# Kernel tuning notes

Measured on AMD Instinct MI355X. Metric: run time of the kernel, lower is better.

## Reference

```python
import jax, jax.numpy as jnp
import numpy as np

N_NODES = 100000
N_EDGES = 3200000
IN_FEATS = 16
OUT_FEATS = 2
K = 3


def setup_inputs() -> dict:
    key = jax.random.key(0)
    k1, k2, k3, k4 = jax.random.split(key, 4)
    in_feat = jax.random.normal(k1, (N_NODES, IN_FEATS), dtype=jnp.float32)
    # Linear(K*in_feats -> out_feats, bias=False) weight, torch layout (out, in)
    W = jax.random.normal(k2, (OUT_FEATS, K * IN_FEATS), dtype=jnp.float32) * (1.0 / np.sqrt(K * IN_FEATS))
    src = jax.random.randint(k3, (N_EDGES,), 0, N_NODES, dtype=jnp.int64)
    dst = jax.random.randint(k4, (N_EDGES,), 0, N_NODES, dtype=jnp.int64)
    # cached dgl.laplacian_lambda_max value; 2.0 is the normalized-Laplacian bound
    lambda_max = jnp.full((1,), 2.0, dtype=jnp.float32)
    return {"in_feat": in_feat, "W": W, "src": src, "dst": dst, "lambda_max": lambda_max}


def reference(in_feat, W, src, dst, lambda_max):
    N = in_feat.shape[0]
    # in-degree based symmetric normalization, clamp(min=1)
    deg = jax.ops.segment_sum(jnp.ones_like(dst, dtype=in_feat.dtype), dst, num_segments=N)
    norm = jnp.clip(deg, 1.0) ** -0.5  # (N,)
    norm = norm[:, None]
    re_norm = (2.0 / lambda_max)[None, :]  # (1,1), broadcasts over nodes

    def prop(x):
        # D^{-1/2} A D^{-1/2} x via gather from src, scatter-sum to dst
        m = (x * norm)[src]                                    # (E, d)
        return jax.ops.segment_sum(m, dst, num_segments=N) * norm

    X0 = in_feat
    X1 = -re_norm * prop(X0) + X0 * (re_norm - 1.0)
    X2 = -2.0 * re_norm * prop(X1) + X1 * (2.0 * (re_norm - 1.0)) - X0
    Xt = jnp.concatenate([X0, X1, X2], axis=1)                 # (N, K*d)
    h = Xt @ W.T                                               # (N, out)
    return jax.nn.relu(h)  # DGL ChebConv default activation
```

## Files before the change

kernel.cpp:

```cpp
#include <hip/hip_runtime.h>
#include <hip/hip_bf16.h>


#define NN   100000
#define NE   3200000
#define F    16
#define CB   128
#define NBUK 782
#define ECHK 8192
#define NBLK 391
#define LCAP 5120
#define HXW  1025

__device__ __forceinline__ float bflo(unsigned int u) {
    return __uint_as_float(u << 16);
}
__device__ __forceinline__ float bfhi(unsigned int u) {
    return __uint_as_float(u & 0xffff0000u);
}
__device__ __forceinline__ unsigned int f2bf(float f) {
    __hip_bfloat16 b = __float2bfloat16(f);
    return (unsigned int)*reinterpret_cast<unsigned short*>(&b);
}

__global__ __launch_bounds__(512) void k_lsort(const int* __restrict__ src,
        const int* __restrict__ dst, int* __restrict__ H, int* __restrict__ hxg,
        int* __restrict__ csort) {
    __shared__ int pk[ECHK];
    __shared__ int hx[HXW];
    __shared__ int cur[1024];
    __shared__ int csum[512];
    int t = threadIdx.x, blk = blockIdx.x;
    for (int j = t; j < 1024; j += 512) hx[j] = 0;
    __syncthreads();
    int s0 = blk * ECHK;
    int lim = min(s0 + ECHK, NE);
    for (int e = s0 + t; e < lim; e += 512)
        atomicAdd(&hx[dst[e] >> 7], 1);
    __syncthreads();
    int b0 = t * 2;
    int c0 = hx[b0], c1 = hx[b0 + 1];
    if (b0 < NBUK)     H[blk * NBUK + b0]     = c0;
    if (b0 + 1 < NBUK) H[blk * NBUK + b0 + 1] = c1;
    csum[t] = c0 + c1;
    __syncthreads();
    for (int o = 1; o < 512; o <<= 1) {
        int add = (t >= o) ? csum[t - o] : 0;
        __syncthreads();
        csum[t] += add;
        __syncthreads();
    }
    int ce = csum[t] - (c0 + c1);
    hx[b0] = ce;  hx[b0 + 1] = ce + c0;
    cur[b0] = ce; cur[b0 + 1] = ce + c0;
    if (t == 511) hx[1024] = csum[511];
    __syncthreads();
    for (int j = t; j < HXW; j += 512)
        hxg[blk * HXW + j] = hx[j];
    for (int e = s0 + t; e < lim; e += 512) {
        int d = dst[e];
        int pos = atomicAdd(&cur[d >> 7], 1);
        pk[pos] = (src[e] << 7) | (d & 127);
    }
    __syncthreads();
    int len = lim - s0;
    for (int i = t; i < len; i += 512)
        csort[s0 + i] = pk[i];
}

__global__ void k_colscan(int* __restrict__ H, int* __restrict__ T) {
    __shared__ int tmp[512];
    int b = blockIdx.x, t = threadIdx.x;
    int v = (t < NBLK) ? H[t * NBUK + b] : 0;
    tmp[t] = v;
    __syncthreads();
    for (int o = 1; o < 512; o <<= 1) {
        int add = (t >= o) ? tmp[t - o] : 0;
        __syncthreads();
        tmp[t] += add;
        __syncthreads();
    }
    if (t < NBLK) H[t * NBUK + b] = tmp[t] - v;
    if (t == 0) T[b] = tmp[511];
}

__global__ void k_basescan(const int* __restrict__ T, int* __restrict__ base) {
    __shared__ int tmp[1024];
    int t = threadIdx.x;
    int v = (t < NBUK) ? T[t] : 0;
    tmp[t] = v;
    __syncthreads();
    for (int o = 1; o < 1024; o <<= 1) {
        int add = (t >= o) ? tmp[t - o] : 0;
        __syncthreads();
        tmp[t] += add;
        __syncthreads();
    }
    if (t < NBUK) base[t] = tmp[t] - v;
    if (t == 0) base[NBUK] = tmp[1023];
}

__global__ __launch_bounds__(256) void k_sort(const int* __restrict__ csort,
        const int* __restrict__ H, const int* __restrict__ hxg,
        const int* __restrict__ base, const float* __restrict__ X0,
        int* __restrict__ es, int* __restrict__ node_off,
        float* __restrict__ norm, unsigned short* __restrict__ Y0) {
    __shared__ int pk[LCAP];
    __shared__ int cnt[CB], loc[CB], cur[CB];
    __shared__ float nvs[CB];
    int b = blockIdx.x, t = threadIdx.x;
    int beg = base[b], end = base[b + 1];
    int len = end - beg;
    if (len > LCAP) len = LCAP;
    if (t < CB) cnt[t] = 0;
    if (b == 0 && t < F) Y0[(size_t)NN * F + t] = 0;
    __syncthreads();
    for (int c = t; c < NBLK; c += 256) {
        int h0 = hxg[c * HXW + b];
        int h1 = hxg[c * HXW + b + 1];
        int dpos = H[c * NBUK + b];
        int rl = h1 - h0;
        if (dpos >= LCAP) continue;
        if (dpos + rl > LCAP) rl = LCAP - dpos;
        int sbase = c * ECHK + h0;
        for (int i = 0; i < rl; ++i)
            pk[dpos + i] = csort[sbase + i];
    }
    __syncthreads();
    for (int i = t; i < len; i += 256)
        atomicAdd(&cnt[pk[i] & 127], 1);
    __syncthreads();
    if (t < CB) loc[t] = cnt[t];
    __syncthreads();
    for (int o = 1; o < CB; o <<= 1) {
        int add = 0;
        if (t < CB && t >= o) add = loc[t - o];
        __syncthreads();
        if (t < CB) loc[t] += add;
        __syncthreads();
    }
    if (t < CB) {
        int excl = loc[t] - cnt[t];
        loc[t] = excl;
        cur[t] = 0;
        int n = b * CB + t;
        if (n <= NN) node_off[n] = beg + excl;
        if (n < NN) {
            int c = cnt[t];
            float nv = rsqrtf((float)(c < 1 ? 1 : c));
            norm[n] = nv;
            nvs[t] = nv;
        }
    }
    __syncthreads();
    for (int j = t; j < CB * F; j += 256) {
        int dl = j >> 4;
        int n = b * CB + dl;
        if (n < NN) {
            size_t gidx = (size_t)n * F + (j & 15);
            Y0[gidx] = (unsigned short)f2bf(X0[gidx] * nvs[dl]);
        }
    }
    for (int i = t; i < len; i += 256) {
        int p = pk[i];
        int dl = p & 127;
        int pos = beg + loc[dl] + atomicAdd(&cur[dl], 1);
        es[pos] = p >> 7;
    }
}

__global__ __launch_bounds__(256) void k_prop1(const int* __restrict__ off,
        const int* __restrict__ es, const unsigned short* __restrict__ Y0,
        const float* __restrict__ X0, const float* __restrict__ norm,
        const float* __restrict__ lm, unsigned short* __restrict__ Y1) {
    int tid = blockIdx.x * 256 + threadIdx.x;
    if (tid < 4) ((uint2*)Y1)[(size_t)NN * 4 + tid] = make_uint2(0u, 0u);
    int n = tid >> 2, h = tid & 3;
    if (n >= NN) return;
    int beg = off[n], end = off[n + 1];
    const uint2* Yv = (const uint2*)Y0;
    float a0 = 0.f, a1 = 0.f, a2 = 0.f, a3 = 0.f;
    int e0 = beg;
    int c = end - e0;
    int iA = (h < c)     ? es[e0 + h]     : NN;
    int iB = (4 + h < c) ? es[e0 + 4 + h] : NN;
    while (e0 < end) {
        int e1 = e0 + 8;
        int c1 = end - e1;
        int nA = (h < c1)     ? es[e1 + h]     : NN;
        int nB = (4 + h < c1) ? es[e1 + 4 + h] : NN;
#pragma unroll
        for (int j = 0; j < 4; ++j) {
            int s = __shfl(iA, j, 4);
            uint2 u = Yv[(size_t)s * 4 + h];
            a0 += bflo(u.x); a1 += bfhi(u.x);
            a2 += bflo(u.y); a3 += bfhi(u.y);
        }
#pragma unroll
        for (int j = 0; j < 4; ++j) {
            int s = __shfl(iB, j, 4);
            uint2 u = Yv[(size_t)s * 4 + h];
            a0 += bflo(u.x); a1 += bfhi(u.x);
            a2 += bflo(u.y); a3 += bfhi(u.y);
        }
        iA = nA; iB = nB; e0 = e1;
    }
    float r  = 2.0f / lm[0];
    float nv = norm[n];
    float k1 = -r * nv, k2 = r - 1.0f;
    float4 x0 = ((const float4*)X0)[tid];
    float x1a = k1 * a0 + k2 * x0.x;
    float x1b = k1 * a1 + k2 * x0.y;
    float x1c = k1 * a2 + k2 * x0.z;
    float x1d = k1 * a3 + k2 * x0.w;
    uint2 o;
    o.x = f2bf(nv * x1a) | (f2bf(nv * x1b) << 16);
    o.y = f2bf(nv * x1c) | (f2bf(nv * x1d) << 16);
    ((uint2*)Y1)[tid] = o;
}

__global__ __launch_bounds__(256) void k_prop2(const int* __restrict__ off,
        const int* __restrict__ es, const unsigned short* __restrict__ Y1,
        const float* __restrict__ X0, const float* __restrict__ norm,
        const float* __restrict__ lm, const float* __restrict__ W,
        float* __restrict__ out) {
    __shared__ float Ws[96];
    if (threadIdx.x < 96) Ws[threadIdx.x] = W[threadIdx.x];
    __syncthreads();
    int tid = blockIdx.x * 256 + threadIdx.x;
    int n = tid >> 2, h = tid & 3;
    if (n >= NN) return;
    int beg = off[n], end = off[n + 1];
    const uint2* Yv = (const uint2*)Y1;
    float a0 = 0.f, a1 = 0.f, a2 = 0.f, a3 = 0.f;
    int e0 = beg;
    int c = end - e0;
    int iA = (h < c)     ? es[e0 + h]     : NN;
    int iB = (4 + h < c) ? es[e0 + 4 + h] : NN;
    while (e0 < end) {
        int e1 = e0 + 8;
        int c1 = end - e1;
        int nA = (h < c1)     ? es[e1 + h]     : NN;
        int nB = (4 + h < c1) ? es[e1 + 4 + h] : NN;
#pragma unroll
        for (int j = 0; j < 4; ++j) {
            int s = __shfl(iA, j, 4);
            uint2 u = Yv[(size_t)s * 4 + h];
            a0 += bflo(u.x); a1 += bfhi(u.x);
            a2 += bflo(u.y); a3 += bfhi(u.y);
        }
#pragma unroll
        for (int j = 0; j < 4; ++j) {
            int s = __shfl(iB, j, 4);
            uint2 u = Yv[(size_t)s * 4 + h];
            a0 += bflo(u.x); a1 += bfhi(u.x);
            a2 += bflo(u.y); a3 += bfhi(u.y);
        }
        iA = nA; iB = nB; e0 = e1;
    }
    float r  = 2.0f / lm[0];
    float nv = norm[n];
    float rn = 1.0f / nv;
    float4 x0 = ((const float4*)X0)[tid];
    uint2 uy = ((const uint2*)Y1)[tid];
    float x1a = bflo(uy.x) * rn, x1b = bfhi(uy.x) * rn;
    float x1c = bflo(uy.y) * rn, x1d = bfhi(uy.y) * rn;
    float c1 = -2.0f * r * nv, c2 = 2.0f * (r - 1.0f);
    float x2a = c1 * a0 + c2 * x1a - x0.x;
    float x2b = c1 * a1 + c2 * x1b - x0.y;
    float x2c = c1 * a2 + c2 * x1c - x0.z;
    float x2d = c1 * a3 + c2 * x1d - x0.w;
    int f0 = 4 * h;
    float t0 = Ws[f0] * x0.x + Ws[f0 + 1] * x0.y + Ws[f0 + 2] * x0.z + Ws[f0 + 3] * x0.w
             + Ws[16 + f0] * x1a + Ws[17 + f0] * x1b + Ws[18 + f0] * x1c + Ws[19 + f0] * x1d
             + Ws[32 + f0] * x2a + Ws[33 + f0] * x2b + Ws[34 + f0] * x2c + Ws[35 + f0] * x2d;
    float t1 = Ws[48 + f0] * x0.x + Ws[49 + f0] * x0.y + Ws[50 + f0] * x0.z + Ws[51 + f0] * x0.w
             + Ws[64 + f0] * x1a + Ws[65 + f0] * x1b + Ws[66 + f0] * x1c + Ws[67 + f0] * x1d
             + Ws[80 + f0] * x2a + Ws[81 + f0] * x2b + Ws[82 + f0] * x2c + Ws[83 + f0] * x2d;
    t0 += __shfl_xor(t0, 2, 4); t0 += __shfl_xor(t0, 1, 4);
    t1 += __shfl_xor(t1, 2, 4); t1 += __shfl_xor(t1, 1, 4);
    if (h == 0) {
        out[(size_t)n * 2 + 0] = fmaxf(t0, 0.f);
        out[(size_t)n * 2 + 1] = fmaxf(t1, 0.f);
    }
}

extern "C" void kernel_launch(void* const* d_in, const int* in_sizes, int n_in,
                              void* d_out, int out_size, void* d_ws, size_t ws_size,
                              hipStream_t stream) {
    const float* X0  = (const float*)d_in[0];
    const float* W   = (const float*)d_in[1];
    const int*   src = (const int*)d_in[2];
    const int*   dst = (const int*)d_in[3];
    const float* lm  = (const float*)d_in[4];
    float* out = (float*)d_out;

    int*   H        = (int*)d_ws;
    int*   hxg      = H + (size_t)NBLK * NBUK;
    int*   T        = hxg + (size_t)NBLK * HXW;
    int*   base     = T + NBUK;
    int*   csort    = base + (NBUK + 1);
    int*   es       = csort + NE;
    int*   node_off = es + NE;
    float* norm     = (float*)(node_off + (NN + 1));
    unsigned short* Y0 = (unsigned short*)(norm + NN);
    unsigned short* Y1 = Y0 + (size_t)(NN + 1) * F;

    const int gridP = (NN * 4 + 255) / 256;

    k_lsort   <<<NBLK, 512, 0, stream>>>(src, dst, H, hxg, csort);
    k_colscan <<<NBUK, 512, 0, stream>>>(H, T);
    k_basescan<<<1, 1024, 0, stream>>>(T, base);
    k_sort    <<<NBUK, 256, 0, stream>>>(csort, H, hxg, base, X0, es, node_off, norm, Y0);
    k_prop1   <<<gridP, 256, 0, stream>>>(node_off, es, Y0, X0, norm, lm, Y1);
    k_prop2   <<<gridP, 256, 0, stream>>>(node_off, es, Y1, X0, norm, lm, W, out);
}
```

Measured before the change: 196.8 us.

## Fuse bucket sort with first propagation and drop global base scan

Removes the global base scan by giving each destination bucket a fixed LCAP-sized slot in the edge array, and packs each node's offset and degree into one word. Degrees are now counted with global atomics during the local sort, so a separate k_norm kernel can build Y0 before the sort. The first propagation is fused into the per-bucket sort kernel and reads sorted indices straight from shared memory. The second propagation stages each half-bucket's edge indices in shared memory. The trade-offs are 3.2M global atomics on deg, an extra memset and launch, a larger padded es array, and degree clamped to 1023 in the packed word.

Result: slower. 318.8 us (+62.0%).

```diff
diff --git a/kernel.cpp b/kernel.cpp
--- a/kernel.cpp
+++ b/kernel.cpp
@@ -11,6 +11,7 @@
 #define NBLK 391
 #define LCAP 5120
 #define HXW  1025
+#define PCAP 4608
 
 __device__ __forceinline__ float bflo(unsigned int u) {
     return __uint_as_float(u << 16);
@@ -25,7 +26,7 @@
 
 __global__ __launch_bounds__(512) void k_lsort(const int* __restrict__ src,
         const int* __restrict__ dst, int* __restrict__ H, int* __restrict__ hxg,
-        int* __restrict__ csort) {
+        int* __restrict__ csort, int* __restrict__ deg) {
     __shared__ int pk[ECHK];
     __shared__ int hx[HXW];
     __shared__ int cur[1024];
@@ -35,8 +36,11 @@
     __syncthreads();
     int s0 = blk * ECHK;
     int lim = min(s0 + ECHK, NE);
-    for (int e = s0 + t; e < lim; e += 512)
-        atomicAdd(&hx[dst[e] >> 7], 1);
+    for (int e = s0 + t; e < lim; e += 512) {
+        int d = dst[e];
+        atomicAdd(&hx[d >> 7], 1);
+        atomicAdd(&deg[d], 1);
+    }
     __syncthreads();
     int b0 = t * 2;
     int c0 = hx[b0], c1 = hx[b0 + 1];
@@ -68,7 +72,7 @@
         csort[s0 + i] = pk[i];
 }
 
-__global__ void k_colscan(int* __restrict__ H, int* __restrict__ T) {
+__global__ void k_colscan(int* __restrict__ H) {
     __shared__ int tmp[512];
     int b = blockIdx.x, t = threadIdx.x;
     int v = (t < NBLK) ? H[t * NBUK + b] : 0;
@@ -81,41 +85,42 @@
         __syncthreads();
     }
     if (t < NBLK) H[t * NBUK + b] = tmp[t] - v;
-    if (t == 0) T[b] = tmp[511];
-}
-
-__global__ void k_basescan(const int* __restrict__ T, int* __restrict__ base) {
-    __shared__ int tmp[1024];
-    int t = threadIdx.x;
-    int v = (t < NBUK) ? T[t] : 0;
-    tmp[t] = v;
-    __syncthreads();
-    for (int o = 1; o < 1024; o <<= 1) {
-        int add = (t >= o) ? tmp[t - o] : 0;
-        __syncthreads();
-        tmp[t] += add;
-        __syncthreads();
-    }
-    if (t < NBUK) base[t] = tmp[t] - v;
-    if (t == 0) base[NBUK] = tmp[1023];
-}
-
-__global__ __launch_bounds__(256) void k_sort(const int* __restrict__ csort,
+}
+
+__global__ __launch_bounds__(256) void k_norm(const int* __restrict__ deg,
+        const float* __restrict__ X0, unsigned short* __restrict__ Y0,
+        unsigned short* __restrict__ Y1) {
+    int tid = blockIdx.x * 256 + threadIdx.x;
+    if (tid < 4) {
+        ((uint2*)Y0)[(size_t)NN * 4 + tid] = make_uint2(0u, 0u);
+        ((uint2*)Y1)[(size_t)NN * 4 + tid] = make_uint2(0u, 0u);
+    }
+    int n = tid >> 2;
+    if (n >= NN) return;
+    int d = deg[n];
+    float nv = rsqrtf((float)(d < 1 ? 1 : d));
+    float4 x0 = ((const float4*)X0)[tid];
+    uint2 o;
+    o.x = f2bf(x0.x * nv) | (f2bf(x0.y * nv) << 16);
+    o.y = f2bf(x0.z * nv) | (f2bf(x0.w * nv) << 16);
+    ((uint2*)Y0)[tid] = o;
+}
+
+__global__ __launch_bounds__(512) void k_sortprop1(const int* __restrict__ csort,
         const int* __restrict__ H, const int* __restrict__ hxg,
-        const int* __restrict__ base, const float* __restrict__ X0,
-        int* __restrict__ es, int* __restrict__ node_off,
-        float* __restrict__ norm, unsigned short* __restrict__ Y0) {
+        const float* __restrict__ X0, const float* __restrict__ lm,
+        int* __restrict__ es, unsigned int* __restrict__ P,
+        const unsigned short* __restrict__ Y0, unsigned short* __restrict__ Y1) {
     __shared__ int pk[LCAP];
+    __shared__ int pk2[LCAP];
     __shared__ int cnt[CB], loc[CB], cur[CB];
-    __shared__ float nvs[CB];
+    __shared__ int lenS;
     int b = blockIdx.x, t = threadIdx.x;
-    int beg = base[b], end = base[b + 1];
-    int len = end - beg;
-    if (len > LCAP) len = LCAP;
     if (t < CB) cnt[t] = 0;
-    if (b == 0 && t < F) Y0[(size_t)NN * F + t] = 0;
-    __syncthreads();
-    for (int c = t; c < NBLK; c += 256) {
+    if (t == 0) lenS = 0;
+    __syncthreads();
+    int mylen = 0;
+    for (int c = t; c < NBLK; c += 512) {
         int h0 = hxg[c * HXW + b];
         int h1 = hxg[c * HXW + b + 1];
         int dpos = H[c * NBUK + b];
@@ -125,9 +130,12 @@
         int sbase = c * ECHK + h0;
         for (int i = 0; i < rl; ++i)
             pk[dpos + i] = csort[sbase + i];
-    }
-    __syncthreads();
-    for (int i = t; i < len; i += 256)
+        mylen = dpos + rl;
+    }
+    if (mylen > 0) atomicMax(&lenS, mylen);
+    __syncthreads();
+    int len = lenS;
+    for (int i = t; i < len; i += 512)
         atomicAdd(&cnt[pk[i] & 127], 1);
     __syncthreads();
     if (t < CB) loc[t] = cnt[t];
@@ -142,73 +150,45 @@
     if (t < CB) {
         int excl = loc[t] - cnt[t];
         loc[t] = excl;
-        cur[t] = 0;
+        cur[t] = excl;
         int n = b * CB + t;
-        if (n <= NN) node_off[n] = beg + excl;
         if (n < NN) {
-            int c = cnt[t];
-            float nv = rsqrtf((float)(c < 1 ? 1 : c));
-            norm[n] = nv;
-            nvs[t] = nv;
+            unsigned dg = cnt[t] > 1023 ? 1023u : (unsigned)cnt[t];
+            P[n] = ((unsigned)(b * LCAP + excl) << 10) | dg;
         }
     }
     __syncthreads();
-    for (int j = t; j < CB * F; j += 256) {
-        int dl = j >> 4;
-        int n = b * CB + dl;
-        if (n < NN) {
-            size_t gidx = (size_t)n * F + (j & 15);
-            Y0[gidx] = (unsigned short)f2bf(X0[gidx] * nvs[dl]);
-        }
-    }
-    for (int i = t; i < len; i += 256) {
+    for (int i = t; i < len; i += 512) {
         int p = pk[i];
-        int dl = p & 127;
-        int pos = beg + loc[dl] + atomicAdd(&cur[dl], 1);
-        es[pos] = p >> 7;
-    }
-}
-
-__global__ __launch_bounds__(256) void k_prop1(const int* __restrict__ off,
-        const int* __restrict__ es, const unsigned short* __restrict__ Y0,
-        const float* __restrict__ X0, const float* __restrict__ norm,
-        const float* __restrict__ lm, unsigned short* __restrict__ Y1) {
-    int tid = blockIdx.x * 256 + threadIdx.x;
-    if (tid < 4) ((uint2*)Y1)[(size_t)NN * 4 + tid] = make_uint2(0u, 0u);
-    int n = tid >> 2, h = tid & 3;
+        int pos = atomicAdd(&cur[p & 127], 1);
+        pk2[pos] = p >> 7;
+    }
+    __syncthreads();
+    for (int i = t; i < len; i += 512)
+        es[b * LCAP + i] = pk2[i];
+    int nl = t >> 2, h = t & 3;
+    int n = b * CB + nl;
     if (n >= NN) return;
-    int beg = off[n], end = off[n + 1];
+    int beg = loc[nl];
+    int lend = beg + cnt[nl];
     const uint2* Yv = (const uint2*)Y0;
     float a0 = 0.f, a1 = 0.f, a2 = 0.f, a3 = 0.f;
-    int e0 = beg;
-    int c = end - e0;
-    int iA = (h < c)     ? es[e0 + h]     : NN;
-    int iB = (4 + h < c) ? es[e0 + 4 + h] : NN;
-    while (e0 < end) {
-        int e1 = e0 + 8;
-        int c1 = end - e1;
-        int nA = (h < c1)     ? es[e1 + h]     : NN;
-        int nB = (4 + h < c1) ? es[e1 + 4 + h] : NN;
+    for (int e0 = beg; e0 < lend; e0 += 8) {
 #pragma unroll
-        for (int j = 0; j < 4; ++j) {
-            int s = __shfl(iA, j, 4);
+        for (int j = 0; j < 8; ++j) {
+            int sp = e0 + j;
+            int s = (sp < lend) ? pk2[sp] : NN;
             uint2 u = Yv[(size_t)s * 4 + h];
             a0 += bflo(u.x); a1 += bfhi(u.x);
             a2 += bflo(u.y); a3 += bfhi(u.y);
         }
-#pragma unroll
-        for (int j = 0; j < 4; ++j) {
-            int s = __shfl(iB, j, 4);
-            uint2 u = Yv[(size_t)s * 4 + h];
-            a0 += bflo(u.x); a1 += bfhi(u.x);
-            a2 += bflo(u.y); a3 += bfhi(u.y);
-        }
-        iA = nA; iB = nB; e0 = e1;
-    }
+    }
+    int dg = cnt[nl];
+    float nv = rsqrtf((float)(dg < 1 ? 1 : dg));
     float r  = 2.0f / lm[0];
-    float nv = norm[n];
     float k1 = -r * nv, k2 = r - 1.0f;
-    float4 x0 = ((const float4*)X0)[tid];
+    int tid4 = n * 4 + h;
+    float4 x0 = ((const float4*)X0)[tid4];
     float x1a = k1 * a0 + k2 * x0.x;
     float x1b = k1 * a1 + k2 * x0.y;
     float x1c = k1 * a2 + k2 * x0.z;
@@ -216,53 +196,54 @@
     uint2 o;
     o.x = f2bf(nv * x1a) | (f2bf(nv * x1b) << 16);
     o.y = f2bf(nv * x1c) | (f2bf(nv * x1d) << 16);
-    ((uint2*)Y1)[tid] = o;
-}
-
-__global__ __launch_bounds__(256) void k_prop2(const int* __restrict__ off,
+    ((uint2*)Y1)[tid4] = o;
+}
+
+__global__ __launch_bounds__(256) void k_prop2(const unsigned int* __restrict__ P,
         const int* __restrict__ es, const unsigned short* __restrict__ Y1,
-        const float* __restrict__ X0, const float* __restrict__ norm,
-        const float* __restrict__ lm, const float* __restrict__ W,
-        float* __restrict__ out) {
+        const float* __restrict__ X0, const float* __restrict__ lm,
+        const float* __restrict__ W, float* __restrict__ out) {
+    __shared__ int sidx[PCAP];
     __shared__ float Ws[96];
-    if (threadIdx.x < 96) Ws[threadIdx.x] = W[threadIdx.x];
-    __syncthreads();
-    int tid = blockIdx.x * 256 + threadIdx.x;
-    int n = tid >> 2, h = tid & 3;
+    int blk = blockIdx.x, t = threadIdx.x;
+    int b = blk >> 1, half = blk & 1;
+    int n0 = b * CB + half * 64;
+    if (n0 >= NN) return;
+    if (t < 96) Ws[t] = W[t];
+    unsigned pk0 = P[n0];
+    int nL = min(n0 + 63, NN - 1);
+    unsigned pkL = P[nL];
+    int st = (int)(pk0 >> 10);
+    int en = (int)(pkL >> 10) + (int)(pkL & 1023u);
+    int slen = en - st;
+    if (slen > PCAP) slen = PCAP;
+    for (int i = t; i < slen; i += 256)
+        sidx[i] = es[st + i];
+    __syncthreads();
+    int n = n0 + (t >> 2), h = t & 3;
     if (n >= NN) return;
-    int beg = off[n], end = off[n + 1];
+    unsigned pkn = P[n];
+    int beg = (int)(pkn >> 10) - st;
+    int dg = (int)(pkn & 1023u);
+    int lend = min(beg + dg, slen);
     const uint2* Yv = (const uint2*)Y1;
     float a0 = 0.f, a1 = 0.f, a2 = 0.f, a3 = 0.f;
-    int e0 = beg;
-    int c = end - e0;
-    int iA = (h < c)     ? es[e0 + h]     : NN;
-    int iB = (4 + h < c) ? es[e0 + 4 + h] : NN;
-    while (e0 < end) {
-        int e1 = e0 + 8;
-        int c1 = end - e1;
-        int nA = (h < c1)     ? es[e1 + h]     : NN;
-        int nB = (4 + h < c1) ? es[e1 + 4 + h] : NN;
+    for (int e0 = beg; e0 < lend; e0 += 8) {
 #pragma unroll
-        for (int j = 0; j < 4; ++j) {
-            int s = __shfl(iA, j, 4);
+        for (int j = 0; j < 8; ++j) {
+            int sp = e0 + j;
+            int s = (sp < lend) ? sidx[sp] : NN;
             uint2 u = Yv[(size_t)s * 4 + h];
             a0 += bflo(u.x); a1 += bfhi(u.x);
             a2 += bflo(u.y); a3 += bfhi(u.y);
         }
-#pragma unroll
-        for (int j = 0; j < 4; ++j) {
-            int s = __shfl(iB, j, 4);
-            uint2 u = Yv[(size_t)s * 4 + h];
-            a0 += bflo(u.x); a1 += bfhi(u.x);
-            a2 += bflo(u.y); a3 += bfhi(u.y);
-        }
-        iA = nA; iB = nB; e0 = e1;
-    }
+    }
+    float nv = rsqrtf((float)(dg < 1 ? 1 : dg));
+    float rn = 1.0f / nv;
     float r  = 2.0f / lm[0];
-    float nv = norm[n];
-    float rn = 1.0f / nv;
-    float4 x0 = ((const float4*)X0)[tid];
-    uint2 uy = ((const uint2*)Y1)[tid];
+    int tid4 = n * 4 + h;
+    float4 x0 = ((const float4*)X0)[tid4];
+    uint2 uy = ((const uint2*)Y1)[tid4];
     float x1a = bflo(uy.x) * rn, x1b = bfhi(uy.x) * rn;
     float x1c = bflo(uy.y) * rn, x1d = bfhi(uy.y) * rn;
     float c1 = -2.0f * r * nv, c2 = 2.0f * (r - 1.0f);
@@ -295,23 +276,19 @@
     const float* lm  = (const float*)d_in[4];
     float* out = (float*)d_out;
 
-    int*   H        = (int*)d_ws;
-    int*   hxg      = H + (size_t)NBLK * NBUK;
-    int*   T        = hxg + (size_t)NBLK * HXW;
-    int*   base     = T + NBUK;
-    int*   csort    = base + (NBUK + 1);
-    int*   es       = csort + NE;
-    int*   node_off = es + NE;
-    float* norm     = (float*)(node_off + (NN + 1));
-    unsigned short* Y0 = (unsigned short*)(norm + NN);
+    int*   H     = (int*)d_ws;
+    int*   hxg   = H + (size_t)NBLK * NBUK;
+    int*   csort = hxg + (size_t)NBLK * HXW;
+    int*   es    = csort + NE;
+    unsigned int* P = (unsigned int*)(es + (size_t)NBUK * LCAP);
+    int*   deg   = (int*)(P + NN);
+    unsigned short* Y0 = (unsigned short*)(deg + NN);
     unsigned short* Y1 = Y0 + (size_t)(NN + 1) * F;
 
-    const int gridP = (NN * 4 + 255) / 256;
-
-    k_lsort   <<<NBLK, 512, 0, stream>>>(src, dst, H, hxg, csort);
-    k_colscan <<<NBUK, 512, 0, stream>>>(H, T);
-    k_basescan<<<1, 1024, 0, stream>>>(T, base);
-    k_sort    <<<NBUK, 256, 0, stream>>>(csort, H, hxg, base, X0, es, node_off, norm, Y0);
-    k_prop1   <<<gridP, 256, 0, stream>>>(node_off, es, Y0, X0, norm, lm, Y1);
-    k_prop2   <<<gridP, 256, 0, stream>>>(node_off, es, Y1, X0, norm, lm, W, out);
-}
+    hipMemsetAsync(deg, 0, NN * sizeof(int), stream);
+    k_lsort    <<<NBLK, 512, 0, stream>>>(src, dst, H, hxg, csort, deg);
+    k_colscan  <<<NBUK, 512, 0, stream>>>(H);
+    k_norm     <<<(NN * 4 + 255) / 256, 256, 0, stream>>>(deg, X0, Y0, Y1);
+    k_sortprop1<<<NBUK, 512, 0, stream>>>(csort, H, hxg, X0, lm, es, P, Y0, Y1);
+    k_prop2    <<<NBUK * 2, 256, 0, stream>>>(P, es, Y1, X0, lm, W, out);
+}
```
